# Kernel optimization log

Hardware: AMD Instinct MI355X
Metric: run time of the kernel (lower is better)

## Reference

```python
import jax, jax.numpy as jnp
import numpy as np

# relations: (source_channel, target_channel, dy_gt, dx_gt, dz_gt)
_RELATIONS = np.array([
    [0, 1,  0.1,  0.0,  0.05],
    [1, 2,  0.0,  0.1,  0.0 ],
    [2, 3, -0.1,  0.05, 0.0 ],
    [3, 4,  0.0,  0.0,  0.1 ],
    [4, 5,  0.05,-0.05, 0.0 ],
    [5, 6,  0.0,  0.1, -0.1 ],
    [6, 7,  0.1,  0.0,  0.0 ],
    [0, 7, -0.05, 0.05, 0.05],
], dtype=np.float32)
REL_I = jnp.asarray(_RELATIONS[:, 0].astype(np.int32))   # [R]
REL_J = jnp.asarray(_RELATIONS[:, 1].astype(np.int32))   # [R]
REL_GT = jnp.asarray(_RELATIONS[:, 2:5])                  # [R, 3] -> (dy, dx, dz)


def setup_inputs() -> dict:
    key = jax.random.key(0)
    output = jax.random.normal(key, (2, 8, 128, 128, 128), dtype=jnp.float32)
    return {"output": output}


def reference(output):
    B, C, H, W, D = output.shape
    # normalized coordinate maps (torch meshgrid 'ij': y over H, x over W, z over D)
    cy = (jnp.arange(H, dtype=output.dtype) / H)[:, None, None]  # [H,1,1]
    cx = (jnp.arange(W, dtype=output.dtype) / W)[None, :, None]  # [1,W,1]
    cz = (jnp.arange(D, dtype=output.dtype) / D)[None, None, :]  # [1,1,D]

    # nn.Threshold(0.5, 0): x if x > 0.5 else 0
    t = jnp.where(output > 0.5, output, jnp.zeros((), output.dtype))  # [B,C,H,W,D]

    s = jnp.sum(t, axis=(2, 3, 4))                 # [B,C]
    centroids_y = jnp.sum(t * cy, axis=(2, 3, 4)) / s  # [B,C]
    centroids_x = jnp.sum(t * cx, axis=(2, 3, 4)) / s  # [B,C]
    centroids_z = jnp.sum(t * cz, axis=(2, 3, 4)) / s  # [B,C]

    # vectorized relation loop: diffs are [B, R]
    dy = centroids_y[:, REL_I] - centroids_y[:, REL_J] - REL_GT[None, :, 0]
    dx = centroids_x[:, REL_I] - centroids_x[:, REL_J] - REL_GT[None, :, 1]
    dz = centroids_z[:, REL_I] - centroids_z[:, REL_J] - REL_GT[None, :, 2]

    def _err(d):  # mean over batch of squared, nan/inf -> 0, then sum over relations
        d = jnp.nan_to_num(d, nan=0.0, posinf=0.0, neginf=0.0)
        return jnp.sum(jnp.mean(jnp.square(d), axis=0))

    return _err(dy) + _err(dx) + _err(dz)
```

## Files before the change

kernel.cpp:

```cpp
#include <hip/hip_runtime.h>
#include <math.h>


#define SLICES 16
#define SLICE_ELEMS (128*128*128)
#define BLOCKS_PER_SLICE 64
#define THREADS 256

__global__ void gsl_init_ws(float* __restrict__ ws) {
    int i = threadIdx.x;
    if (i < SLICES * 4) ws[i] = 0.0f;
}

__global__ __launch_bounds__(THREADS)
void gsl_reduce(const float* __restrict__ in, float* __restrict__ ws) {
    const int slice = blockIdx.y;
    const float4* p = reinterpret_cast<const float4*>(in + (size_t)slice * SLICE_ELEMS);
    const int tid = threadIdx.x;
    const int nvec = SLICE_ELEMS / 4;
    const int stride = BLOCKS_PER_SLICE * THREADS;

    float s = 0.0f, sy = 0.0f, sx = 0.0f, sz = 0.0f;

    for (int v = blockIdx.x * THREADS + tid; v < nvec; v += stride) {
        float4 f = p[v];
        int e = v << 2;
        float t0 = f.x > 0.5f ? f.x : 0.0f;
        float t1 = f.y > 0.5f ? f.y : 0.0f;
        float t2 = f.z > 0.5f ? f.z : 0.0f;
        float t3 = f.w > 0.5f ? f.w : 0.0f;
        float ts = (t0 + t1) + (t2 + t3);
        float zz = (float)(e & 127);
        float xx = (float)((e >> 7) & 127);
        float yy = (float)(e >> 14);
        s  += ts;
        sy += ts * yy;
        sx += ts * xx;
        sz += ts * zz + (t1 + 2.0f * t2 + 3.0f * t3);
    }

    const float inv = 1.0f / 128.0f;
    sy *= inv; sx *= inv; sz *= inv;

    #pragma unroll
    for (int off = 32; off > 0; off >>= 1) {
        s  += __shfl_down(s,  off, 64);
        sy += __shfl_down(sy, off, 64);
        sx += __shfl_down(sx, off, 64);
        sz += __shfl_down(sz, off, 64);
    }

    __shared__ float sh[4][4];
    const int wave = tid >> 6;
    const int lane = tid & 63;
    if (lane == 0) {
        sh[wave][0] = s; sh[wave][1] = sy; sh[wave][2] = sx; sh[wave][3] = sz;
    }
    __syncthreads();
    if (tid == 0) {
        float a = 0.0f, b = 0.0f, c = 0.0f, d = 0.0f;
        #pragma unroll
        for (int w = 0; w < 4; ++w) {
            a += sh[w][0]; b += sh[w][1]; c += sh[w][2]; d += sh[w][3];
        }
        atomicAdd(&ws[slice * 4 + 0], a);
        atomicAdd(&ws[slice * 4 + 1], b);
        atomicAdd(&ws[slice * 4 + 2], c);
        atomicAdd(&ws[slice * 4 + 3], d);
    }
}

__global__ void gsl_finalize(const float* __restrict__ ws, float* __restrict__ out) {
    if (threadIdx.x != 0 || blockIdx.x != 0) return;

    float cy[SLICES], cx[SLICES], cz[SLICES];
    for (int i = 0; i < SLICES; ++i) {
        float s = ws[i * 4 + 0];
        cy[i] = ws[i * 4 + 1] / s;
        cx[i] = ws[i * 4 + 2] / s;
        cz[i] = ws[i * 4 + 3] / s;
    }

    const int   ri[8] = {0, 1, 2, 3, 4, 5, 6, 0};
    const int   rj[8] = {1, 2, 3, 4, 5, 6, 7, 7};
    const float gy[8] = { 0.1f, 0.0f, -0.1f, 0.0f,  0.05f, 0.0f, 0.1f, -0.05f};
    const float gx[8] = { 0.0f, 0.1f,  0.05f, 0.0f, -0.05f, 0.1f, 0.0f,  0.05f};
    const float gz[8] = { 0.05f, 0.0f, 0.0f,  0.1f,  0.0f, -0.1f, 0.0f,  0.05f};

    float loss = 0.0f;
    for (int r = 0; r < 8; ++r) {
        for (int b = 0; b < 2; ++b) {
            int i = b * 8 + ri[r];
            int j = b * 8 + rj[r];
            float dy = cy[i] - cy[j] - gy[r];
            float dx = cx[i] - cx[j] - gx[r];
            float dz = cz[i] - cz[j] - gz[r];
            if (!isfinite(dy)) dy = 0.0f;
            if (!isfinite(dx)) dx = 0.0f;
            if (!isfinite(dz)) dz = 0.0f;
            loss += 0.5f * (dy * dy + dx * dx + dz * dz);
        }
    }
    out[0] = loss;
}

extern "C" void kernel_launch(void* const* d_in, const int* in_sizes, int n_in,
                              void* d_out, int out_size, void* d_ws, size_t ws_size,
                              hipStream_t stream) {
    const float* in = (const float*)d_in[0];
    float* out = (float*)d_out;
    float* ws = (float*)d_ws;

    gsl_init_ws<<<1, 64, 0, stream>>>(ws);
    gsl_reduce<<<dim3(BLOCKS_PER_SLICE, SLICES), THREADS, 0, stream>>>(in, ws);
    gsl_finalize<<<1, 64, 0, stream>>>(ws, out);
}
```

Baseline: 212.8 us.

## Replace atomics with per-block partials, drop init kernel, unroll fixed-trip load loop

Each block now writes its four partial sums to its own workspace slot instead of atomically adding into a shared per-slice accumulator, so the zero-init kernel launch is removed. The finalize kernel sums the 64 partials per slice in parallel with shuffles before the relation loss is computed on one thread. The main loop gets a compile-time trip count of 32 with unroll 8 to expose more outstanding loads. This saves one launch and the atomics, at the cost of a slightly larger finalize reduction. It depends on the workspace holding 1024 float4 values.

```diff
diff --git a/kernel.cpp b/kernel.cpp
--- a/kernel.cpp
+++ b/kernel.cpp
@@ -6,25 +6,23 @@
 #define SLICE_ELEMS (128*128*128)
 #define BLOCKS_PER_SLICE 64
 #define THREADS 256
-
-__global__ void gsl_init_ws(float* __restrict__ ws) {
-    int i = threadIdx.x;
-    if (i < SLICES * 4) ws[i] = 0.0f;
-}
+#define NVEC (SLICE_ELEMS / 4)
+#define STRIDE (BLOCKS_PER_SLICE * THREADS)
 
 __global__ __launch_bounds__(THREADS)
-void gsl_reduce(const float* __restrict__ in, float* __restrict__ ws) {
+void gsl_reduce(const float* __restrict__ in, float4* __restrict__ ws4) {
     const int slice = blockIdx.y;
     const float4* p = reinterpret_cast<const float4*>(in + (size_t)slice * SLICE_ELEMS);
     const int tid = threadIdx.x;
-    const int nvec = SLICE_ELEMS / 4;
-    const int stride = BLOCKS_PER_SLICE * THREADS;
+    const int base = blockIdx.x * THREADS + tid;
 
     float s = 0.0f, sy = 0.0f, sx = 0.0f, sz = 0.0f;
 
-    for (int v = blockIdx.x * THREADS + tid; v < nvec; v += stride) {
+    #pragma unroll 8
+    for (int i = 0; i < 32; ++i) {
+        const int v = base + i * STRIDE;
         float4 f = p[v];
-        int e = v << 2;
+        const int e = v << 2;
         float t0 = f.x > 0.5f ? f.x : 0.0f;
         float t1 = f.y > 0.5f ? f.y : 0.0f;
         float t2 = f.z > 0.5f ? f.z : 0.0f;
@@ -50,58 +48,74 @@
         sz += __shfl_down(sz, off, 64);
     }
 
-    __shared__ float sh[4][4];
+    __shared__ float4 sh[4];
     const int wave = tid >> 6;
     const int lane = tid & 63;
-    if (lane == 0) {
-        sh[wave][0] = s; sh[wave][1] = sy; sh[wave][2] = sx; sh[wave][3] = sz;
-    }
+    if (lane == 0) sh[wave] = make_float4(s, sy, sx, sz);
     __syncthreads();
     if (tid == 0) {
-        float a = 0.0f, b = 0.0f, c = 0.0f, d = 0.0f;
-        #pragma unroll
-        for (int w = 0; w < 4; ++w) {
-            a += sh[w][0]; b += sh[w][1]; c += sh[w][2]; d += sh[w][3];
-        }
-        atomicAdd(&ws[slice * 4 + 0], a);
-        atomicAdd(&ws[slice * 4 + 1], b);
-        atomicAdd(&ws[slice * 4 + 2], c);
-        atomicAdd(&ws[slice * 4 + 3], d);
+        float4 a = sh[0], b = sh[1], c = sh[2], d = sh[3];
+        float4 r = make_float4((a.x + b.x) + (c.x + d.x),
+                               (a.y + b.y) + (c.y + d.y),
+                               (a.z + b.z) + (c.z + d.z),
+                               (a.w + b.w) + (c.w + d.w));
+        ws4[slice * BLOCKS_PER_SLICE + blockIdx.x] = r;
     }
 }
 
-__global__ void gsl_finalize(const float* __restrict__ ws, float* __restrict__ out) {
-    if (threadIdx.x != 0 || blockIdx.x != 0) return;
+__global__ __launch_bounds__(THREADS)
+void gsl_finalize(const float4* __restrict__ ws4, float* __restrict__ out) {
+    const int t = threadIdx.x;
+    const int slice = t >> 4;
+    const int chunk = t & 15;
 
-    float cy[SLICES], cx[SLICES], cz[SLICES];
-    for (int i = 0; i < SLICES; ++i) {
-        float s = ws[i * 4 + 0];
-        cy[i] = ws[i * 4 + 1] / s;
-        cx[i] = ws[i * 4 + 2] / s;
-        cz[i] = ws[i * 4 + 3] / s;
+    float s = 0.0f, sy = 0.0f, sx = 0.0f, sz = 0.0f;
+    #pragma unroll
+    for (int i = 0; i < 4; ++i) {
+        float4 f = ws4[slice * BLOCKS_PER_SLICE + chunk * 4 + i];
+        s += f.x; sy += f.y; sx += f.z; sz += f.w;
+    }
+    #pragma unroll
+    for (int off = 8; off > 0; off >>= 1) {
+        s  += __shfl_down(s,  off, 16);
+        sy += __shfl_down(sy, off, 16);
+        sx += __shfl_down(sx, off, 16);
+        sz += __shfl_down(sz, off, 16);
     }
 
-    const int   ri[8] = {0, 1, 2, 3, 4, 5, 6, 0};
-    const int   rj[8] = {1, 2, 3, 4, 5, 6, 7, 7};
-    const float gy[8] = { 0.1f, 0.0f, -0.1f, 0.0f,  0.05f, 0.0f, 0.1f, -0.05f};
-    const float gx[8] = { 0.0f, 0.1f,  0.05f, 0.0f, -0.05f, 0.1f, 0.0f,  0.05f};
-    const float gz[8] = { 0.05f, 0.0f, 0.0f,  0.1f,  0.0f, -0.1f, 0.0f,  0.05f};
+    __shared__ float cy[SLICES], cx[SLICES], cz[SLICES];
+    if (chunk == 0) {
+        cy[slice] = sy / s;
+        cx[slice] = sx / s;
+        cz[slice] = sz / s;
+    }
+    __syncthreads();
 
-    float loss = 0.0f;
-    for (int r = 0; r < 8; ++r) {
-        for (int b = 0; b < 2; ++b) {
-            int i = b * 8 + ri[r];
-            int j = b * 8 + rj[r];
-            float dy = cy[i] - cy[j] - gy[r];
-            float dx = cx[i] - cx[j] - gx[r];
-            float dz = cz[i] - cz[j] - gz[r];
-            if (!isfinite(dy)) dy = 0.0f;
-            if (!isfinite(dx)) dx = 0.0f;
-            if (!isfinite(dz)) dz = 0.0f;
-            loss += 0.5f * (dy * dy + dx * dx + dz * dz);
+    if (t == 0) {
+        const int   ri[8] = {0, 1, 2, 3, 4, 5, 6, 0};
+        const int   rj[8] = {1, 2, 3, 4, 5, 6, 7, 7};
+        const float gy[8] = { 0.1f, 0.0f, -0.1f, 0.0f,  0.05f, 0.0f, 0.1f, -0.05f};
+        const float gx[8] = { 0.0f, 0.1f,  0.05f, 0.0f, -0.05f, 0.1f, 0.0f,  0.05f};
+        const float gz[8] = { 0.05f, 0.0f, 0.0f,  0.1f,  0.0f, -0.1f, 0.0f,  0.05f};
+
+        float loss = 0.0f;
+        #pragma unroll
+        for (int r = 0; r < 8; ++r) {
+            #pragma unroll
+            for (int b = 0; b < 2; ++b) {
+                int i = b * 8 + ri[r];
+                int j = b * 8 + rj[r];
+                float dy = cy[i] - cy[j] - gy[r];
+                float dx = cx[i] - cx[j] - gx[r];
+                float dz = cz[i] - cz[j] - gz[r];
+                if (!isfinite(dy)) dy = 0.0f;
+                if (!isfinite(dx)) dx = 0.0f;
+                if (!isfinite(dz)) dz = 0.0f;
+                loss += 0.5f * (dy * dy + dx * dx + dz * dz);
+            }
         }
+        out[0] = loss;
     }
-    out[0] = loss;
 }
 
 extern "C" void kernel_launch(void* const* d_in, const int* in_sizes, int n_in,
@@ -109,9 +123,8 @@
                               hipStream_t stream) {
     const float* in = (const float*)d_in[0];
     float* out = (float*)d_out;
-    float* ws = (float*)d_ws;
+    float4* ws4 = (float4*)d_ws;
 
-    gsl_init_ws<<<1, 64, 0, stream>>>(ws);
-    gsl_reduce<<<dim3(BLOCKS_PER_SLICE, SLICES), THREADS, 0, stream>>>(in, ws);
-    gsl_finalize<<<1, 64, 0, stream>>>(ws, out);
+    gsl_reduce<<<dim3(BLOCKS_PER_SLICE, SLICES), THREADS, 0, stream>>>(in, ws4);
+    gsl_finalize<<<1, THREADS, 0, stream>>>(ws4, out);
 }
```

Result: faster. 192.5 us (-9.5%).
